# Kernel optimization log

Measured on AMD Instinct MI355X. Metric: run time of the kernel, lower is better.

The kernel has to match this reference:

```python
import jax, jax.numpy as jnp
import numpy as np
import math

N, C_IN, H, W = 8, 64, 128, 128
C_OUT, K = 128, 5
MU = 0.9

def _masks():
    _mu = (1.0 - MU) / 3.0
    neighbor = jnp.array([
        [0, _mu, 0, _mu, 0],
        [_mu, _mu, _mu, _mu, _mu],
        [0, _mu, 0, _mu, 0],
        [_mu, _mu, _mu, _mu, _mu],
        [0, _mu, 0, _mu, 0]], dtype=jnp.float32)
    dilator = jnp.array([
        [1.0, 0.0, 1.0, 0.0, 1.0],
        [0.0, 0.0, 0.0, 0.0, 0.0],
        [1.0, 0.0, 1.0, 0.0, 1.0],
        [0.0, 0.0, 0.0, 0.0, 0.0],
        [1.0, 0.0, 1.0, 0.0, 1.0]], dtype=jnp.float32)
    return neighbor, dilator

def setup_inputs() -> dict:
    key = jax.random.key(0)
    k1, k2 = jax.random.split(key)
    input_ = jax.random.normal(k1, (N, C_IN, H, W), dtype=jnp.float32)
    stdv = 1.0 / math.sqrt(C_IN * K * K)
    weight = jax.random.uniform(k2, (C_OUT, C_IN, K, K), dtype=jnp.float32,
                                minval=-stdv, maxval=stdv)
    return {"input_": input_, "weight": weight}

def reference(input_, weight):
    # Faithful math: f_kernel = weight * dilator_mask + neighbor_weight_mask,
    # then a standard 5x5 conv (stride=1, pad=2, dilation=1). The original
    # realizes the conv via F.unfold + matmul (im2col); conv_general_dilated
    # computes identical values. Bias exists as a parameter but is never
    # applied in the original forward, so it is omitted here.
    neighbor, dilator = _masks()
    f_kernel = weight * dilator + neighbor  # broadcast over (O, I)
    out = jax.lax.conv_general_dilated(
        input_, f_kernel,
        window_strides=(1, 1),
        padding=((2, 2), (2, 2)),
        rhs_dilation=(1, 1),
        dimension_numbers=("NCHW", "OIHW", "NCHW"))
    return out  # [N, C_OUT, H, W]
```

## Files before the change

kernel.cpp:

```cpp
#include <hip/hip_runtime.h>

typedef short short8 __attribute__((ext_vector_type(8)));
typedef float f32x4 __attribute__((ext_vector_type(4)));
typedef float f32x2 __attribute__((ext_vector_type(2)));

#define NN 8
#define CI 64
#define CO 128
#define HH 128
#define WW 128
#define PH 132
#define PW 132
#define MU 0.033333333333333333f

#define WS_W_BYTES (9 * 128 * 64 * 2)
#define WS_T_OFF   WS_W_BYTES
#define WS_T_BYTES (NN * PH * PW * 4)
#define WS_X_OFF   (WS_T_OFF + WS_T_BYTES)
#define WS_X_BYTES ((size_t)NN * PH * PW * CI * 2)
#define WS_NB_OFF  (WS_X_OFF + WS_X_BYTES)
#define WS_TOTAL   (WS_NB_OFF + WS_T_BYTES)

__device__ __forceinline__ unsigned short f2bf(float f) {
  unsigned u = __float_as_uint(f);
  u += 0x7fffu + ((u >> 16) & 1u);
  return (unsigned short)(u >> 16);
}

__device__ __forceinline__ void g2lds16(const void* g, void* l) {
  __builtin_amdgcn_global_load_lds(
      (const __attribute__((address_space(1))) unsigned int*)g,
      (__attribute__((address_space(3))) unsigned int*)l, 16, 0, 0);
}
__device__ __forceinline__ void g2lds4(const void* g, void* l) {
  __builtin_amdgcn_global_load_lds(
      (const __attribute__((address_space(1))) unsigned int*)g,
      (__attribute__((address_space(3))) unsigned int*)l, 4, 0, 0);
}

__global__ __launch_bounds__(256) void prep_kernel(
    const float* __restrict__ in, const float* __restrict__ w,
    unsigned short* __restrict__ ws_w, float* __restrict__ ws_T,
    short8* __restrict__ ws_x) {
  const int b = blockIdx.x, tid = threadIdx.x;
  if (b < 256) {
    __shared__ short8 lx[512][8];
    const int n = b >> 5, quad = b & 31;
    const int rl = tid >> 6;
    const int x2 = (tid & 63) * 2;
    const int r = quad * 4 + rl;
    const float* src = in + ((size_t)(n * CI) * HH + r) * WW + x2;
    const int px0 = rl * 128 + x2;
    float ts0 = 0.f, ts1 = 0.f;
    #pragma unroll
    for (int g = 0; g < 8; ++g) {
      short8 pk0, pk1;
      #pragma unroll
      for (int j = 0; j < 8; ++j) {
        const f32x2 v = *(const f32x2*)(src + (size_t)(g * 8 + j) * (HH * WW));
        ts0 += v[0]; ts1 += v[1];
        pk0[j] = (short)f2bf(v[0]);
        pk1[j] = (short)f2bf(v[1]);
      }
      lx[px0][g ^ (px0 & 7)] = pk0;
      lx[px0 + 1][g ^ ((px0 + 1) & 7)] = pk1;
    }
    *(f32x2*)&ws_T[(n * PH + r + 2) * PW + (x2 + 2)] = (f32x2){ts0, ts1};
    __syncthreads();
    #pragma unroll
    for (int it = 0; it < 16; ++it) {
      const int G = it * 256 + tid;
      const int px2 = G >> 3, g2 = G & 7;
      const int r2 = quad * 4 + (px2 >> 7), x2b = px2 & 127;
      ws_x[((size_t)(n * PH + r2 + 2) * PW + (x2b + 2)) * 8 + g2] =
          lx[px2][g2 ^ (px2 & 7)];
    }
  } else if (b < 264) {
    const int n = b - 256;
    const short8 z = {0, 0, 0, 0, 0, 0, 0, 0};
    for (int e = tid; e < 1040 * 8; e += 256) {
      const int px = e >> 3, g = e & 7;
      int y, x;
      if (px < 528) { const int r4 = px / 132; y = (r4 < 2) ? r4 : r4 + 128; x = px - r4 * 132; }
      else { const int q = px - 528; const int c4 = q >> 7; x = (c4 < 2) ? c4 : c4 + 128; y = 2 + (q & 127); }
      ws_x[((size_t)(n * PH + y) * PW + x) * 8 + g] = z;
    }
    for (int e = tid; e < 1040; e += 256) {
      int y, x;
      if (e < 528) { const int r4 = e / 132; y = (r4 < 2) ? r4 : r4 + 128; x = e - r4 * 132; }
      else { const int q = e - 528; const int c4 = q >> 7; x = (c4 < 2) ? c4 : c4 + 128; y = 2 + (q & 127); }
      ws_T[(n * PH + y) * PW + x] = 0.f;
    }
  } else {
    const int el = (b - 264) * 256 + tid;
    const int lane = el & 63;
    const int idx = el >> 6;
    const int ks = idx & 1, cb = (idx >> 1) & 7, tap = idx >> 4;
    const int lo = lane & 15, hi = lane >> 4;
    const int ky = (tap / 3) * 2, kx = (tap % 3) * 2;
    const float* wp = w + (size_t)((cb * 16 + lo) * 64 + ks * 32 + hi * 8) * 25
                        + ky * 5 + kx;
    short8 pk;
    #pragma unroll
    for (int j = 0; j < 8; ++j) pk[j] = (short)f2bf(wp[j * 25]);
    ((short8*)ws_w)[el] = pk;
  }
}

__global__ __launch_bounds__(256) void nb_kernel(
    const float* __restrict__ ws_T, float* __restrict__ ws_nb) {
  const int p = blockIdx.x * 256 + threadIdx.x;
  const int n = p >> 14, yx = p & 16383;
  const int y = yx >> 7, x = yx & 127;
  const float* Tb = ws_T + (size_t)(n * PH + y) * PW + x;
  float s = 0.f;
  #pragma unroll
  for (int ky = 0; ky < 5; ++ky)
    #pragma unroll
    for (int kx = 0; kx < 5; ++kx)
      if ((ky & 1) | (kx & 1)) s += Tb[ky * PW + kx];
  ws_nb[(size_t)p] = s * MU;
}

__global__ __launch_bounds__(256)
__attribute__((amdgpu_waves_per_eu(2, 2)))
void conv_kernel(
    const unsigned short* __restrict__ ws_w, const float* __restrict__ ws_nb,
    const unsigned short* __restrict__ ws_x, float* __restrict__ out) {
  __shared__ short8 halo[288 * 8];
  __shared__ float  nbt[128];

  const int tid = threadIdx.x;
  const int wave = tid >> 6, lane = tid & 63;
  const int bid = blockIdx.x;
  const int n = bid & 7;
  const int rest = bid >> 3;
  const int cob = rest & 3;
  const int Y0 = (rest >> 2) * 8;
  const int lo = lane & 15, hi = lane >> 4;

  const short8* wsv = (const short8*)ws_w;
  short8 W[36];
  #pragma unroll
  for (int k = 0; k < 36; ++k)
    W[k] = wsv[((k >> 2) * 16 + cob * 4 + (k & 3)) * 64 + lane];

  for (int j = 0; j < 8; ++j) {
    const int ty0 = Y0 + (j >> 2) * 4;
    const int tx0 = (j & 3) * 32;

    for (int k = wave; k < 36; k += 4) {
      const int pos = k * 8 + (lane >> 3);
      const int r = pos / 36, c = pos - r * 36;
      const int chunk = (lane & 7) ^ (pos & 7);
      const unsigned short* g =
          ws_x + ((size_t)(n * PH + ty0 + r) * PW + (tx0 + c)) * 64 + chunk * 8;
      g2lds16(g, (char*)halo + k * 1024);
    }
    if (wave < 2) {
      const float* g = ws_nb
          + (size_t)((n * 128 + ty0 + 2 * wave + (lane >> 5)) * 128)
          + tx0 + (lane & 31);
      g2lds4(g, (char*)nbt + wave * 256);
    }
    __syncthreads();

    const f32x4 nbv0 = *(const f32x4*)&nbt[wave * 32 + 0  + hi * 4];
    const f32x4 nbv1 = *(const f32x4*)&nbt[wave * 32 + 16 + hi * 4];
    f32x4 acc00 = nbv0, acc01 = nbv1;
    f32x4 acc10 = nbv0, acc11 = nbv1;

    short8 Aaf0, Aaf1;
    short8 Baf0, Baf1;
    short8 Caf0, Caf1;

#define LOADSET(P, K) { \
      constexpr int tap_ = (K) >> 1, ks_ = (K) & 1; \
      constexpr int ty_ = (tap_ / 3) * 2, tx_ = (tap_ % 3) * 2; \
      const int p0_ = (wave + ty_) * 36 + (lo + tx_); \
      const int p1_ = p0_ + 16; \
      P##af0 = halo[p0_ * 8 + ((ks_ * 4 + hi) ^ (p0_ & 7))]; \
      P##af1 = halo[p1_ * 8 + ((ks_ * 4 + hi) ^ (p1_ & 7))]; \
    }
#define MFMASET(P, K) { \
      constexpr int tap_ = (K) >> 1, ks_ = (K) & 1; \
      acc00 = __builtin_amdgcn_mfma_f32_16x16x32_bf16(P##af0, W[tap_ * 4 + 0 + ks_], acc00, 0, 0, 0); \
      acc01 = __builtin_amdgcn_mfma_f32_16x16x32_bf16(P##af1, W[tap_ * 4 + 0 + ks_], acc01, 0, 0, 0); \
      acc10 = __builtin_amdgcn_mfma_f32_16x16x32_bf16(P##af0, W[tap_ * 4 + 2 + ks_], acc10, 0, 0, 0); \
      acc11 = __builtin_amdgcn_mfma_f32_16x16x32_bf16(P##af1, W[tap_ * 4 + 2 + ks_], acc11, 0, 0, 0); \
    }

    LOADSET(A, 0); LOADSET(B, 1);
    LOADSET(C, 2);  MFMASET(A, 0);
    LOADSET(A, 3);  MFMASET(B, 1);
    LOADSET(B, 4);  MFMASET(C, 2);
    LOADSET(C, 5);  MFMASET(A, 3);
    LOADSET(A, 6);  MFMASET(B, 4);
    LOADSET(B, 7);  MFMASET(C, 5);
    LOADSET(C, 8);  MFMASET(A, 6);
    LOADSET(A, 9);  MFMASET(B, 7);
    LOADSET(B, 10); MFMASET(C, 8);
    LOADSET(C, 11); MFMASET(A, 9);
    LOADSET(A, 12); MFMASET(B, 10);
    LOADSET(B, 13); MFMASET(C, 11);
    LOADSET(C, 14); MFMASET(A, 12);
    LOADSET(A, 15); MFMASET(B, 13);
    LOADSET(B, 16); MFMASET(C, 14);
    LOADSET(C, 17); MFMASET(A, 15);
    MFMASET(B, 16);
    MFMASET(C, 17);
#undef LOADSET
#undef MFMASET

    {
      const int gy = ty0 + wave;
      const int gx0 = tx0 + hi * 4;
      const int co0 = cob * 32 + lo;
      *(f32x4*)&out[(((size_t)n * CO + co0) * HH + gy) * WW + gx0] = acc00;
      *(f32x4*)&out[(((size_t)n * CO + co0) * HH + gy) * WW + gx0 + 16] = acc01;
      *(f32x4*)&out[(((size_t)n * CO + co0 + 16) * HH + gy) * WW + gx0] = acc10;
      *(f32x4*)&out[(((size_t)n * CO + co0 + 16) * HH + gy) * WW + gx0 + 16] = acc11;
    }
    __syncthreads();
  }
}

__global__ __launch_bounds__(256) void prep_kernel_safe(
    const float* __restrict__ in, const float* __restrict__ w,
    unsigned short* __restrict__ ws_w, float* __restrict__ ws_T) {
  const int bid = blockIdx.x, tid = threadIdx.x;
  if (bid < 288) {
    const int el = bid * 256 + tid;
    const int tap = el >> 13;
    const int rem = el & 8191;
    const int co = rem >> 6, ic = rem & 63;
    const int ky = (tap / 3) * 2, kx = (tap % 3) * 2;
    ws_w[el] = f2bf(w[(co * 64 + ic) * 25 + ky * 5 + kx]);
  } else {
    const int p = (bid - 288) * 256 + tid;
    const int n = p >> 14;
    const int yx = p & 16383;
    const float* base = in + (size_t)n * CI * (HH * WW) + yx;
    float s = 0.f;
    #pragma unroll
    for (int ic = 0; ic < CI; ++ic) s += base[ic * (HH * WW)];
    ws_T[p] = s;
  }
}

#define SHR 12
#define SHC 36
#define SNPOS (SHR * SHC)

__global__ __launch_bounds__(256, 2) void conv_kernel_safe(
    const float* __restrict__ in, const unsigned short* __restrict__ ws_w,
    const float* __restrict__ ws_T, float* __restrict__ out) {
  __shared__ short8 in_lds[SNPOS * 8];
  __shared__ float T_lds[SNPOS];

  const int tid = threadIdx.x;
  const int t = blockIdx.x;
  const int n = blockIdx.y;
  const int ty0 = (t >> 2) * 8;
  const int tx0 = (t & 3) * 32;

  for (int e = tid; e < SNPOS * 8; e += 256) {
    const int slot = e / SNPOS;
    const int pos = e - slot * SNPOS;
    const int r = pos / SHC, c = pos - r * SHC;
    const int gy = ty0 + r - 2, gx = tx0 + c - 2;
    const bool ok = (gy >= 0 && gy < HH && gx >= 0 && gx < WW);
    const long off = ((long)(n * CI + slot * 8) * HH + gy) * WW + gx;
    short8 pk;
    #pragma unroll
    for (int j = 0; j < 8; ++j) {
      const float v = ok ? in[off + (long)j * (HH * WW)] : 0.f;
      pk[j] = (short)f2bf(v);
    }
    in_lds[pos * 8 + (slot ^ (pos & 7))] = pk;
  }
  for (int e = tid; e < SNPOS; e += 256) {
    const int r = e / SHC, c = e - r * SHC;
    const int gy = ty0 + r - 2, gx = tx0 + c - 2;
    T_lds[e] = (gy >= 0 && gy < HH && gx >= 0 && gx < WW)
                   ? ws_T[((size_t)n * HH + gy) * WW + gx] : 0.f;
  }
  __syncthreads();

  const int wave = tid >> 6;
  const int lane = tid & 63;
  const int lo = lane & 15;
  const int hi = lane >> 4;

  int py[4], pxc[4];
  #pragma unroll
  for (int f = 0; f < 4; ++f) {
    const int pb = wave * 64 + f * 16;
    py[f] = pb >> 5;
    pxc[f] = (pb & 31) + lo;
  }

  f32x4 acc[8][4];
  #pragma unroll
  for (int cb = 0; cb < 8; ++cb)
    #pragma unroll
    for (int f = 0; f < 4; ++f) acc[cb][f] = (f32x4){0.f, 0.f, 0.f, 0.f};

  const short8* wsv = (const short8*)ws_w;

  #pragma unroll
  for (int tap = 0; tap < 9; ++tap) {
    const int ty = (tap / 3) * 2, tx = (tap % 3) * 2;
    #pragma unroll
    for (int ks = 0; ks < 2; ++ks) {
      short8 bfrag[4];
      #pragma unroll
      for (int f = 0; f < 4; ++f) {
        const int pos = (py[f] + ty) * SHC + (pxc[f] + tx);
        bfrag[f] = in_lds[pos * 8 + ((ks * 4 + hi) ^ (pos & 7))];
      }
      #pragma unroll
      for (int cb = 0; cb < 8; ++cb) {
        const short8 afrag = wsv[(tap * 128 + cb * 16 + lo) * 8 + ks * 4 + hi];
        #pragma unroll
        for (int f = 0; f < 4; ++f)
          acc[cb][f] = __builtin_amdgcn_mfma_f32_16x16x32_bf16(
              afrag, bfrag[f], acc[cb][f], 0, 0, 0);
      }
    }
  }

  float nb[4];
  #pragma unroll
  for (int f = 0; f < 4; ++f) {
    float s = 0.f;
    #pragma unroll
    for (int ky = 0; ky < 5; ++ky)
      #pragma unroll
      for (int kx = 0; kx < 5; ++kx)
        if ((ky & 1) | (kx & 1))
          s += T_lds[(py[f] + ky) * SHC + (pxc[f] + kx)];
    nb[f] = s * MU;
  }

  #pragma unroll
  for (int cb = 0; cb < 8; ++cb) {
    #pragma unroll
    for (int f = 0; f < 4; ++f) {
      const int gy = ty0 + py[f];
      const int gx = tx0 + pxc[f];
      #pragma unroll
      for (int q = 0; q < 4; ++q) {
        const int co = cb * 16 + hi * 4 + q;
        out[(((size_t)n * CO + co) * HH + gy) * WW + gx] = acc[cb][f][q] + nb[f];
      }
    }
  }
}

extern "C" void kernel_launch(void* const* d_in, const int* in_sizes, int n_in,
                              void* d_out, int out_size, void* d_ws, size_t ws_size,
                              hipStream_t stream) {
  const float* in = (const float*)d_in[0];
  const float* w  = (const float*)d_in[1];
  float* out = (float*)d_out;
  unsigned short* ws_w = (unsigned short*)d_ws;

  if (ws_size >= WS_TOTAL) {
    float* ws_T = (float*)((char*)d_ws + WS_T_OFF);
    short8* ws_x = (short8*)((char*)d_ws + WS_X_OFF);
    float* ws_nb = (float*)((char*)d_ws + WS_NB_OFF);
    prep_kernel<<<dim3(300), 256, 0, stream>>>(in, w, ws_w, ws_T, ws_x);
    nb_kernel<<<dim3(512), 256, 0, stream>>>(ws_T, ws_nb);
    conv_kernel<<<dim3(512), 256, 0, stream>>>(
        ws_w, ws_nb, (const unsigned short*)ws_x, out);
  } else {
    float* ws_T = (float*)((char*)d_ws + WS_W_BYTES);
    prep_kernel_safe<<<dim3(288 + 512), 256, 0, stream>>>(in, w, ws_w, ws_T);
    conv_kernel_safe<<<dim3(64, NN), 256, 0, stream>>>(in, ws_w, ws_T, out);
  }
}
```

Before: 43.67 us.

## Enlarge conv tile to 8 rows per iteration with two rows per wave

Result: no change. 43.93 us (+0.6%).

```diff
diff --git a/kernel.cpp b/kernel.cpp
--- a/kernel.cpp
+++ b/kernel.cpp
@@ -127,8 +127,8 @@
 void conv_kernel(
     const unsigned short* __restrict__ ws_w, const float* __restrict__ ws_nb,
     const unsigned short* __restrict__ ws_x, float* __restrict__ out) {
-  __shared__ short8 halo[288 * 8];
-  __shared__ float  nbt[128];
+  __shared__ short8 halo[432 * 8];
+  __shared__ float  nbt[256];
 
   const int tid = threadIdx.x;
   const int wave = tid >> 6, lane = tid & 63;
@@ -145,81 +145,97 @@
   for (int k = 0; k < 36; ++k)
     W[k] = wsv[((k >> 2) * 16 + cob * 4 + (k & 3)) * 64 + lane];
 
-  for (int j = 0; j < 8; ++j) {
-    const int ty0 = Y0 + (j >> 2) * 4;
-    const int tx0 = (j & 3) * 32;
-
-    for (int k = wave; k < 36; k += 4) {
+  for (int j = 0; j < 4; ++j) {
+    const int tx0 = j * 32;
+
+    for (int k = wave; k < 54; k += 4) {
       const int pos = k * 8 + (lane >> 3);
       const int r = pos / 36, c = pos - r * 36;
       const int chunk = (lane & 7) ^ (pos & 7);
       const unsigned short* g =
-          ws_x + ((size_t)(n * PH + ty0 + r) * PW + (tx0 + c)) * 64 + chunk * 8;
+          ws_x + ((size_t)(n * PH + Y0 + r) * PW + (tx0 + c)) * 64 + chunk * 8;
       g2lds16(g, (char*)halo + k * 1024);
     }
-    if (wave < 2) {
+    {
       const float* g = ws_nb
-          + (size_t)((n * 128 + ty0 + 2 * wave + (lane >> 5)) * 128)
+          + (size_t)((n * 128 + Y0 + 2 * wave + (lane >> 5)) * 128)
           + tx0 + (lane & 31);
       g2lds4(g, (char*)nbt + wave * 256);
     }
     __syncthreads();
 
-    const f32x4 nbv0 = *(const f32x4*)&nbt[wave * 32 + 0  + hi * 4];
-    const f32x4 nbv1 = *(const f32x4*)&nbt[wave * 32 + 16 + hi * 4];
-    f32x4 acc00 = nbv0, acc01 = nbv1;
-    f32x4 acc10 = nbv0, acc11 = nbv1;
-
-    short8 Aaf0, Aaf1;
-    short8 Baf0, Baf1;
-    short8 Caf0, Caf1;
+    f32x4 a000, a001, a010, a011;
+    f32x4 a100, a101, a110, a111;
+    {
+      const f32x4 n00 = *(const f32x4*)&nbt[(wave * 2 + 0) * 32 + 0  + hi * 4];
+      const f32x4 n01 = *(const f32x4*)&nbt[(wave * 2 + 0) * 32 + 16 + hi * 4];
+      const f32x4 n10 = *(const f32x4*)&nbt[(wave * 2 + 1) * 32 + 0  + hi * 4];
+      const f32x4 n11 = *(const f32x4*)&nbt[(wave * 2 + 1) * 32 + 16 + hi * 4];
+      a000 = n00; a001 = n01; a010 = n10; a011 = n11;
+      a100 = n00; a101 = n01; a110 = n10; a111 = n11;
+    }
+
+    short8 Aaf00, Aaf01, Aaf10, Aaf11;
+    short8 Baf00, Baf01, Baf10, Baf11;
 
 #define LOADSET(P, K) { \
       constexpr int tap_ = (K) >> 1, ks_ = (K) & 1; \
       constexpr int ty_ = (tap_ / 3) * 2, tx_ = (tap_ % 3) * 2; \
-      const int p0_ = (wave + ty_) * 36 + (lo + tx_); \
-      const int p1_ = p0_ + 16; \
-      P##af0 = halo[p0_ * 8 + ((ks_ * 4 + hi) ^ (p0_ & 7))]; \
-      P##af1 = halo[p1_ * 8 + ((ks_ * 4 + hi) ^ (p1_ & 7))]; \
+      const int q0_ = (wave * 2 + 0 + ty_) * 36 + (lo + tx_); \
+      const int q1_ = q0_ + 36; \
+      P##af00 = halo[q0_ * 8 + ((ks_ * 4 + hi) ^ (q0_ & 7))]; \
+      P##af01 = halo[(q0_ + 16) * 8 + ((ks_ * 4 + hi) ^ ((q0_ + 16) & 7))]; \
+      P##af10 = halo[q1_ * 8 + ((ks_ * 4 + hi) ^ (q1_ & 7))]; \
+      P##af11 = halo[(q1_ + 16) * 8 + ((ks_ * 4 + hi) ^ ((q1_ + 16) & 7))]; \
     }
 #define MFMASET(P, K) { \
       constexpr int tap_ = (K) >> 1, ks_ = (K) & 1; \
-      acc00 = __builtin_amdgcn_mfma_f32_16x16x32_bf16(P##af0, W[tap_ * 4 + 0 + ks_], acc00, 0, 0, 0); \
-      acc01 = __builtin_amdgcn_mfma_f32_16x16x32_bf16(P##af1, W[tap_ * 4 + 0 + ks_], acc01, 0, 0, 0); \
-      acc10 = __builtin_amdgcn_mfma_f32_16x16x32_bf16(P##af0, W[tap_ * 4 + 2 + ks_], acc10, 0, 0, 0); \
-      acc11 = __builtin_amdgcn_mfma_f32_16x16x32_bf16(P##af1, W[tap_ * 4 + 2 + ks_], acc11, 0, 0, 0); \
-    }
-
-    LOADSET(A, 0); LOADSET(B, 1);
-    LOADSET(C, 2);  MFMASET(A, 0);
-    LOADSET(A, 3);  MFMASET(B, 1);
-    LOADSET(B, 4);  MFMASET(C, 2);
-    LOADSET(C, 5);  MFMASET(A, 3);
-    LOADSET(A, 6);  MFMASET(B, 4);
-    LOADSET(B, 7);  MFMASET(C, 5);
-    LOADSET(C, 8);  MFMASET(A, 6);
-    LOADSET(A, 9);  MFMASET(B, 7);
-    LOADSET(B, 10); MFMASET(C, 8);
-    LOADSET(C, 11); MFMASET(A, 9);
-    LOADSET(A, 12); MFMASET(B, 10);
-    LOADSET(B, 13); MFMASET(C, 11);
-    LOADSET(C, 14); MFMASET(A, 12);
-    LOADSET(A, 15); MFMASET(B, 13);
-    LOADSET(B, 16); MFMASET(C, 14);
-    LOADSET(C, 17); MFMASET(A, 15);
-    MFMASET(B, 16);
-    MFMASET(C, 17);
+      const short8 w0_ = W[tap_ * 4 + 0 + ks_]; \
+      const short8 w1_ = W[tap_ * 4 + 2 + ks_]; \
+      a000 = __builtin_amdgcn_mfma_f32_16x16x32_bf16(P##af00, w0_, a000, 0, 0, 0); \
+      a001 = __builtin_amdgcn_mfma_f32_16x16x32_bf16(P##af01, w0_, a001, 0, 0, 0); \
+      a010 = __builtin_amdgcn_mfma_f32_16x16x32_bf16(P##af10, w0_, a010, 0, 0, 0); \
+      a011 = __builtin_amdgcn_mfma_f32_16x16x32_bf16(P##af11, w0_, a011, 0, 0, 0); \
+      a100 = __builtin_amdgcn_mfma_f32_16x16x32_bf16(P##af00, w1_, a100, 0, 0, 0); \
+      a101 = __builtin_amdgcn_mfma_f32_16x16x32_bf16(P##af01, w1_, a101, 0, 0, 0); \
+      a110 = __builtin_amdgcn_mfma_f32_16x16x32_bf16(P##af10, w1_, a110, 0, 0, 0); \
+      a111 = __builtin_amdgcn_mfma_f32_16x16x32_bf16(P##af11, w1_, a111, 0, 0, 0); \
+    }
+
+    LOADSET(A, 0);  LOADSET(B, 1);
+    MFMASET(A, 0);  LOADSET(A, 2);
+    MFMASET(B, 1);  LOADSET(B, 3);
+    MFMASET(A, 2);  LOADSET(A, 4);
+    MFMASET(B, 3);  LOADSET(B, 5);
+    MFMASET(A, 4);  LOADSET(A, 6);
+    MFMASET(B, 5);  LOADSET(B, 7);
+    MFMASET(A, 6);  LOADSET(A, 8);
+    MFMASET(B, 7);  LOADSET(B, 9);
+    MFMASET(A, 8);  LOADSET(A, 10);
+    MFMASET(B, 9);  LOADSET(B, 11);
+    MFMASET(A, 10); LOADSET(A, 12);
+    MFMASET(B, 11); LOADSET(B, 13);
+    MFMASET(A, 12); LOADSET(A, 14);
+    MFMASET(B, 13); LOADSET(B, 15);
+    MFMASET(A, 14); LOADSET(A, 16);
+    MFMASET(B, 15); LOADSET(B, 17);
+    MFMASET(A, 16);
+    MFMASET(B, 17);
 #undef LOADSET
 #undef MFMASET
 
     {
-      const int gy = ty0 + wave;
+      const int gy0 = Y0 + wave * 2;
       const int gx0 = tx0 + hi * 4;
       const int co0 = cob * 32 + lo;
-      *(f32x4*)&out[(((size_t)n * CO + co0) * HH + gy) * WW + gx0] = acc00;
-      *(f32x4*)&out[(((size_t)n * CO + co0) * HH + gy) * WW + gx0 + 16] = acc01;
-      *(f32x4*)&out[(((size_t)n * CO + co0 + 16) * HH + gy) * WW + gx0] = acc10;
-      *(f32x4*)&out[(((size_t)n * CO + co0 + 16) * HH + gy) * WW + gx0 + 16] = acc11;
+      float* o00 = &out[(((size_t)n * CO + co0) * HH + gy0) * WW + gx0];
+      float* o01 = &out[(((size_t)n * CO + co0) * HH + gy0 + 1) * WW + gx0];
+      float* o10 = &out[(((size_t)n * CO + co0 + 16) * HH + gy0) * WW + gx0];
+      float* o11 = &out[(((size_t)n * CO + co0 + 16) * HH + gy0 + 1) * WW + gx0];
+      *(f32x4*)(o00) = a000;      *(f32x4*)(o00 + 16) = a001;
+      *(f32x4*)(o01) = a010;      *(f32x4*)(o01 + 16) = a011;
+      *(f32x4*)(o10) = a100;      *(f32x4*)(o10 + 16) = a101;
+      *(f32x4*)(o11) = a110;      *(f32x4*)(o11 + 16) = a111;
     }
     __syncthreads();
   }
```
